# Performance work log

Measured on AMD Instinct MI355X. Metric: run time of the kernel, lower is better.

Reference implementation:

```python
import jax, jax.numpy as jnp
import numpy as np
import math

D_MODEL = 768
H = 12
D_FF = 3072
HEAD_DIM = D_MODEL // H
EPS = 1e-5


def setup_inputs() -> dict:
    key = jax.random.key(0)
    ks = jax.random.split(key, 12)
    s = 1.0 / math.sqrt(D_MODEL)
    inp = {
        "x": jax.random.normal(ks[0], (8, 1024, D_MODEL), dtype=jnp.float32),
        # attention projections (stored as [d_in, d_out])
        "wq": jax.random.normal(ks[1], (D_MODEL, D_MODEL), jnp.float32) * s,
        "bq": jnp.zeros((D_MODEL,), jnp.float32),
        "wk": jax.random.normal(ks[2], (D_MODEL, D_MODEL), jnp.float32) * s,
        "bk": jnp.zeros((D_MODEL,), jnp.float32),
        "wv": jax.random.normal(ks[3], (D_MODEL, D_MODEL), jnp.float32) * s,
        "bv": jnp.zeros((D_MODEL,), jnp.float32),
        "wo": jax.random.normal(ks[4], (D_MODEL, D_MODEL), jnp.float32) * s,
        "bo": jnp.zeros((D_MODEL,), jnp.float32),
        # FFN
        "w1": jax.random.normal(ks[5], (D_MODEL, D_FF), jnp.float32) * s,
        "b1": jnp.zeros((D_FF,), jnp.float32),
        "w2": jax.random.normal(ks[6], (D_FF, D_MODEL), jnp.float32) * (1.0 / math.sqrt(D_FF)),
        "b2": jnp.zeros((D_MODEL,), jnp.float32),
        # LayerNormalization scalar params (gemma/beta) for the two residual norms
        "g1": jnp.ones((1,), jnp.float32),
        "be1": jnp.zeros((1,), jnp.float32),
        "g2": jnp.ones((1,), jnp.float32),
        "be2": jnp.zeros((1,), jnp.float32),
    }
    return inp


def _layernorm(x, g, b):
    # torch: mean and UNBIASED std over last dim; divide by (std + eps)
    mean = jnp.mean(x, axis=-1, keepdims=True)
    std = jnp.std(x, axis=-1, keepdims=True, ddof=1)
    return g * (x - mean) / (std + EPS) + b


def _attention(x, wq, bq, wk, bk, wv, bv, wo, bo):
    B, N, _ = x.shape
    q = (x @ wq + bq).reshape(B, N, H, HEAD_DIM)
    k = (x @ wk + bk).reshape(B, N, H, HEAD_DIM)
    v = (x @ wv + bv).reshape(B, N, H, HEAD_DIM)
    scores = jnp.einsum("bqhd,bkhd->bhqk", q, k) / math.sqrt(HEAD_DIM)
    w = jax.nn.softmax(scores, axis=-1)
    out = jnp.einsum("bhqk,bkhd->bqhd", w, v).reshape(B, N, D_MODEL)
    return out @ wo + bo


def _ffn(x, w1, b1, w2, b2):
    return (jax.nn.gelu(x @ w1 + b1, approximate=False)) @ w2 + b2


def reference(x, wq, bq, wk, bk, wv, bv, wo, bo, w1, b1, w2, b2, g1, be1, g2, be2):
    # pre-LN residual block 1: attention
    x = x + _attention(_layernorm(x, g1, be1), wq, bq, wk, bk, wv, bv, wo, bo)
    # pre-LN residual block 2: FFN
    x = x + _ffn(_layernorm(x, g2, be2), w1, b1, w2, b2)
    return x
```

## Files before the change

### kernel.cpp

```cpp
#include <hip/hip_runtime.h>
#include <hip/hip_bf16.h>
#include <math.h>

typedef unsigned short u16;
typedef unsigned int u32;
typedef u16 u16x8 __attribute__((ext_vector_type(8)));
typedef __bf16 bf16x8 __attribute__((ext_vector_type(8)));
typedef float f32x4 __attribute__((ext_vector_type(4)));

#define MODE_GELU 1
#define MODE_RESF32 2
#define MODE_QKV 3

template <typename T, typename F>
__device__ __forceinline__ T bitcast(F f) { return __builtin_bit_cast(T, f); }

__device__ __forceinline__ u16 f2bf(float f) {
    unsigned int u = __float_as_uint(f);
    u = (u + 0x7fffu + ((u >> 16) & 1u)) >> 16;
    return (u16)u;
}

__device__ __forceinline__ u32 packbf(float lo, float hi) {
    return (u32)f2bf(lo) | ((u32)f2bf(hi) << 16);
}

__device__ __forceinline__ float fast_gelu(float x) {
    const float arg = x * (2.30220775f + 0.10294329f * x * x);
    const float e = exp2f(arg);
    return x * (1.0f - __builtin_amdgcn_rcpf(e + 1.0f));
}

__device__ __forceinline__ void gl_lds16(const u16* g, u16* l) {
    __builtin_amdgcn_global_load_lds(
        (const __attribute__((address_space(1))) unsigned int*)(const void*)g,
        (__attribute__((address_space(3))) unsigned int*)(void*)l,
        16, 0, 0);
}

__device__ __forceinline__ void stage64(const u16* __restrict__ src, int stride,
                                        u16* __restrict__ lds, int t)
{
    const int wave = t >> 6, lane = t & 63;
#pragma unroll
    for (int i = 0; i < 2; i++) {
        const int row = i * 32 + wave * 8 + (lane >> 3);
        const int s = lane & 7;
        const int f = (((row >> 3) & 1) << 2) | (row & 3);
        gl_lds16(src + (size_t)row * stride + (size_t)((s ^ f) << 3),
                 lds + i * 2048 + wave * 512);
    }
}

__global__ __launch_bounds__(256) void prep_kernel(
    const float* __restrict__ wq, const float* __restrict__ wk,
    const float* __restrict__ wv, const float* __restrict__ wo,
    const float* __restrict__ w1, const float* __restrict__ w2,
    const float* __restrict__ bq, const float* __restrict__ bk,
    const float* __restrict__ bv,
    u16* __restrict__ wqkvT, u16* __restrict__ woT,
    u16* __restrict__ w1T, u16* __restrict__ w2T, float* __restrict__ bqkv,
    const float* __restrict__ X, u16* __restrict__ Y,
    const float* __restrict__ gp, const float* __restrict__ bp)
{
    const int blk = blockIdx.x;
    if (blk >= 6921) {
        __shared__ float sbuf[8];
        const int row = blk - 6921, t = threadIdx.x;
        const float* xr = X + (size_t)row * 768;
        float v0 = xr[t], v1 = xr[t + 256], v2 = xr[t + 512];
        float s = v0 + v1 + v2;
        float q = v0 * v0 + v1 * v1 + v2 * v2;
#pragma unroll
        for (int m = 1; m < 64; m <<= 1) {
            s += __shfl_xor(s, m, 64);
            q += __shfl_xor(q, m, 64);
        }
        const int wave = t >> 6, lane = t & 63;
        if (lane == 0) { sbuf[wave] = s; sbuf[4 + wave] = q; }
        __syncthreads();
        s = sbuf[0] + sbuf[1] + sbuf[2] + sbuf[3];
        q = sbuf[4] + sbuf[5] + sbuf[6] + sbuf[7];
        const float mean = s * (1.0f / 768.0f);
        float ssd = fmaxf(q - 768.0f * mean * mean, 0.0f);
        const float stdv = sqrtf(ssd * (1.0f / 767.0f));
        const float scale = gp[0] / (stdv + 1e-5f);
        const float beta = bp[0];
        u16* yr = Y + (size_t)row * 768;
        yr[t]       = f2bf((v0 - mean) * scale + beta);
        yr[t + 256] = f2bf((v1 - mean) * scale + beta);
        yr[t + 512] = f2bf((v2 - mean) * scale + beta);
        return;
    }
    if (blk >= 6912) {
        const int t = (blk - 6912) * 256 + threadIdx.x;
        if (t < 2304)
            bqkv[t] = t < 768 ? bq[t] : (t < 1536 ? bk[t - 768] : bv[t - 1536]);
        return;
    }
    const float* W; u16* WT; int Krows, Ncols, lt;
    if (blk < 576)       { W = wq; WT = wqkvT;                       Krows = 768;  Ncols = 768;  lt = blk; }
    else if (blk < 1152) { W = wk; WT = wqkvT + (size_t)768 * 768;   Krows = 768;  Ncols = 768;  lt = blk - 576; }
    else if (blk < 1728) { W = wv; WT = wqkvT + (size_t)1536 * 768;  Krows = 768;  Ncols = 768;  lt = blk - 1152; }
    else if (blk < 2304) { W = wo; WT = woT;                         Krows = 768;  Ncols = 768;  lt = blk - 1728; }
    else if (blk < 4608) { W = w1; WT = w1T;                         Krows = 768;  Ncols = 3072; lt = blk - 2304; }
    else                 { W = w2; WT = w2T;                         Krows = 3072; Ncols = 768;  lt = blk - 4608; }
    const int ktiles = Krows >> 5;
    const int k0 = (lt % ktiles) * 32, n0 = (lt / ktiles) * 32;

    __shared__ float tile[32][33];
    const int tx = threadIdx.x & 31, ty = threadIdx.x >> 5;
#pragma unroll
    for (int j = 0; j < 32; j += 8)
        tile[ty + j][tx] = W[(size_t)(k0 + ty + j) * Ncols + n0 + tx];
    __syncthreads();
#pragma unroll
    for (int j = 0; j < 32; j += 8)
        WT[(size_t)(n0 + ty + j) * Krows + k0 + tx] = f2bf(tile[tx][ty + j]);
}

__global__ __launch_bounds__(256) void ln_kernel(
    const float* __restrict__ X, u16* __restrict__ Y,
    const float* __restrict__ gp, const float* __restrict__ bp)
{
    __shared__ float sbuf[8];
    const int row = blockIdx.x, t = threadIdx.x;
    const float* xr = X + (size_t)row * 768;
    float v0 = xr[t], v1 = xr[t + 256], v2 = xr[t + 512];
    float s = v0 + v1 + v2;
    float q = v0 * v0 + v1 * v1 + v2 * v2;
#pragma unroll
    for (int m = 1; m < 64; m <<= 1) {
        s += __shfl_xor(s, m, 64);
        q += __shfl_xor(q, m, 64);
    }
    const int wave = t >> 6, lane = t & 63;
    if (lane == 0) { sbuf[wave] = s; sbuf[4 + wave] = q; }
    __syncthreads();
    s = sbuf[0] + sbuf[1] + sbuf[2] + sbuf[3];
    q = sbuf[4] + sbuf[5] + sbuf[6] + sbuf[7];
    const float mean = s * (1.0f / 768.0f);
    float ssd = fmaxf(q - 768.0f * mean * mean, 0.0f);
    const float stdv = sqrtf(ssd * (1.0f / 767.0f));
    const float scale = gp[0] / (stdv + 1e-5f);
    const float beta = bp[0];
    u16* yr = Y + (size_t)row * 768;
    yr[t]       = f2bf((v0 - mean) * scale + beta);
    yr[t + 256] = f2bf((v1 - mean) * scale + beta);
    yr[t + 512] = f2bf((v2 - mean) * scale + beta);
}

template <int MODE>
__global__ __launch_bounds__(256) void gemm_kernel(
    const u16* __restrict__ A, const u16* __restrict__ BT,
    const float* __restrict__ bias, const float* __restrict__ res,
    void* __restrict__ out0, void* __restrict__ out1, void* __restrict__ out2,
    int M, int N, int K)
{
    __shared__ u16 sh[2][2][128 * 64];
    u16* shp = &sh[0][0][0];
    const int t = threadIdx.x;
    const int lane = t & 63, wave = t >> 6;
    const int wr = wave >> 1, wc = wave & 1;
    const int g = lane >> 4, c = lane & 15;
    const int bm = blockIdx.x, bn = blockIdx.y;

    const int srow = wave * 32 + (lane >> 3);
    const u16* Ag = A + (size_t)(bm * 128 + srow) * K;
    const u16* Bg = BT + (size_t)(bn * 128 + srow) * K;

    const int fc = (((c >> 3) & 1) << 2) | (c & 3);
    const int xs0 = (g ^ fc) << 3;
    const int xs1 = ((4 + g) ^ fc) << 3;

    f32x4 acc[4][4] = {};
    const int nk = K >> 6;

    const int sl = lane & 7;
    int sco[4];
#pragma unroll
    for (int it = 0; it < 4; it++)
        sco[it] = ((sl ^ (((it & 1) << 2) | ((lane >> 3) & 3))) << 3);

#define STAGE_AB(buf, k0)                                                     \
    {                                                                         \
        _Pragma("unroll")                                                     \
        for (int it = 0; it < 4; it++) {                                      \
            gl_lds16(Ag + (size_t)(it * 8) * K + (k0) + sco[it], &sh[buf][0][wave * 2048 + it * 512]); \
            gl_lds16(Bg + (size_t)(it * 8) * K + (k0) + sco[it], &sh[buf][1][wave * 2048 + it * 512]); \
        }                                                                     \
    }

    STAGE_AB(0, 0);
    __syncthreads();

    for (int ks = 0; ks < nk; ks++) {
        const int cur = ks & 1;
        if (ks + 1 < nk) STAGE_AB(cur ^ 1, (ks + 1) << 6);
        const u16* Asb = sh[cur][0];
        const u16* Bsb = sh[cur][1];
        __builtin_amdgcn_s_setprio(1);
#pragma unroll
        for (int kk = 0; kk < 2; kk++) {
            const int xo = kk ? xs1 : xs0;
            bf16x8 af[4], bfr[4];
#pragma unroll
            for (int m = 0; m < 4; m++)
                af[m] = *(const bf16x8*)&Asb[(wr * 64 + m * 16 + c) * 64 + xo];
#pragma unroll
            for (int n = 0; n < 4; n++)
                bfr[n] = *(const bf16x8*)&Bsb[(wc * 64 + n * 16 + c) * 64 + xo];
#pragma unroll
            for (int m = 0; m < 4; m++)
#pragma unroll
                for (int n = 0; n < 4; n++)
                    acc[m][n] = __builtin_amdgcn_mfma_f32_16x16x32_bf16(
                        af[m], bfr[n], acc[m][n], 0, 0, 0);
        }
        __builtin_amdgcn_s_setprio(0);
        __syncthreads();
    }
#undef STAGE_AB

    if constexpr (MODE == MODE_QKV) {
        if (bn >= 12) {
#pragma unroll
            for (int m = 0; m < 4; m++) {
#pragma unroll
                for (int n = 0; n < 4; n++) {
                    const int colL = wc * 64 + n * 16 + c;
                    const int rowLb = wr * 64 + m * 16 + 4 * g;
                    const float bv = bias[bn * 128 + colL];
                    const u32 x0 = packbf(acc[m][n][0] + bv, acc[m][n][1] + bv);
                    const u32 x1 = packbf(acc[m][n][2] + bv, acc[m][n][3] + bv);
                    const int elem = colL * 128 + (rowLb ^ ((colL & 15) << 3));
                    ((u32*)shp)[elem >> 1] = x0;
                    ((u32*)shp)[(elem >> 1) + 1] = x1;
                }
            }
            __syncthreads();
            const int bn_off = bn - 12;
            const int bb = bm >> 3, kvb = (bm & 7) * 128;
            const int j8 = (t & 7) * 8;
#pragma unroll
            for (int it = 0; it < 4; it++) {
                const int colL2 = it * 32 + (t >> 3);
                const int gcol = bn_off * 128 + colL2;
                const int hh = gcol >> 6, d = gcol & 63;
                const size_t obase = ((size_t)(bb * 12 + hh) << 16) + ((size_t)d << 10) + kvb;
                const int X = (colL2 & 15) << 3;
#pragma unroll
                for (int half = 0; half < 2; half++) {
                    const int rowL2 = half * 64 + j8;
                    const int elem = colL2 * 128 + (rowL2 ^ X);
                    *(u16x8*)((u16*)out2 + obase + rowL2) = *(const u16x8*)&shp[elem];
                }
            }
            return;
        }
    }

#pragma unroll
    for (int m = 0; m < 4; m++) {
        const int row = bm * 128 + wr * 64 + m * 16 + 4 * g;
#pragma unroll
        for (int n = 0; n < 4; n++) {
            const int col = bn * 128 + wc * 64 + n * 16 + c;
            const float bv = bias[col];
#pragma unroll
            for (int i = 0; i < 4; i++) {
                float v = acc[m][n][i] + bv;
                if constexpr (MODE == MODE_GELU) {
                    ((u16*)out0)[(size_t)(row + i) * N + col] = f2bf(fast_gelu(v));
                } else if constexpr (MODE == MODE_RESF32) {
                    const size_t idx = (size_t)(row + i) * N + col;
                    ((float*)out0)[idx] = v + res[idx];
                } else {
                    const int sect = (col >= 768) ? 1 : 0;
                    const int colm = col - sect * 768;
                    u16* dst = sect ? (u16*)out1 : (u16*)out0;
                    dst[(size_t)(row + i) * 768 + colm] = f2bf(v);
                }
            }
        }
    }
}

__global__ __launch_bounds__(256) void attn_kernel(
    const u16* __restrict__ Qg, const u16* __restrict__ Kg,
    const u16* __restrict__ Vt_g, u16* __restrict__ O)
{
    __shared__ u16 Kl[2][4096];
    __shared__ u16 Vl[2][4096];
    const int t = threadIdx.x, lane = t & 63, wave = t >> 6;
    const int g = lane >> 4, c = lane & 15;
    const int l = blockIdx.x;
    const int pos = l >> 3;
    const int b = l & 7, h = pos >> 4;
    const int qt = pos & 15;
    const int bh = b * 12 + h;
    const size_t rowb = (size_t)b * 1024;
    const int q0 = qt * 64 + wave * 16;

    bf16x8 qa[2];
    {
        const u16* qp = Qg + (rowb + q0 + c) * 768 + h * 64 + g * 8;
        u16x8 a0 = *(const u16x8*)qp;
        u16x8 a1 = *(const u16x8*)(qp + 32);
        bf16x8 va0, va1;
#pragma unroll
        for (int j = 0; j < 8; j++) {
            const float SC = 0.18033688011112042f;
            va0[j] = (__bf16)(__uint_as_float(((u32)a0[j]) << 16) * SC);
            va1[j] = (__bf16)(__uint_as_float(((u32)a1[j]) << 16) * SC);
        }
        qa[0] = va0; qa[1] = va1;
    }

    int kro[4], kxo[4], vro[4];
#pragma unroll
    for (int n = 0; n < 4; n++) {
        const int pr = ((n >> 1) << 5) + ((c >> 2) << 3) + ((n & 1) << 2) + (c & 3);
        kro[n] = pr << 6;
        kxo[n] = (((pr >> 3) & 1) << 2) | (pr & 3);
        vro[n] = (n * 16 + c) << 6;
    }
    const int vxo = (((c >> 3) & 1) << 2) | (c & 3);

    const u16* ksrc = Kg + rowb * 768 + h * 64;
    const u16* vsrc = Vt_g + (size_t)bh * 65536;

    float m0 = -1e30f, l0 = 0.f;
    f32x4 oa[4] = {};
    const int srcb = (lane & 48) | ((lane >> 2) & 12);

    stage64(ksrc, 768, Kl[0], t);
    stage64(vsrc, 1024, Vl[0], t);
    __syncthreads();

    for (int kvt = 0; kvt < 16; ++kvt) {
        const u16* Kc = Kl[kvt & 1];
        const u16* Vc = Vl[kvt & 1];
        if (kvt < 15) {
            stage64(ksrc + (size_t)(kvt + 1) * 64 * 768, 768, Kl[(kvt + 1) & 1], t);
            stage64(vsrc + (kvt + 1) * 64, 1024, Vl[(kvt + 1) & 1], t);
        }

        f32x4 s0[4] = {};
        __builtin_amdgcn_s_setprio(1);
#pragma unroll
        for (int n = 0; n < 4; n++) {
#pragma unroll
            for (int kk = 0; kk < 2; kk++) {
                const bf16x8 kf = *(const bf16x8*)&Kc[kro[n] + ((((kk << 2) + g) ^ kxo[n]) << 3)];
                s0[n] = __builtin_amdgcn_mfma_f32_16x16x32_bf16(kf, qa[kk], s0[n], 0, 0, 0);
            }
        }
        __builtin_amdgcn_s_setprio(0);

        bf16x8 pa00, pa01;
        {
            float t0 = fmaxf(fmaxf(s0[0][0], s0[0][1]), fmaxf(s0[0][2], s0[0][3]));
            float t1 = fmaxf(fmaxf(s0[1][0], s0[1][1]), fmaxf(s0[1][2], s0[1][3]));
            float t2 = fmaxf(fmaxf(s0[2][0], s0[2][1]), fmaxf(s0[2][2], s0[2][3]));
            float t3 = fmaxf(fmaxf(s0[3][0], s0[3][1]), fmaxf(s0[3][2], s0[3][3]));
            float mx = fmaxf(fmaxf(t0, t1), fmaxf(t2, t3));
            mx = fmaxf(mx, __shfl_xor(mx, 16, 64));
            mx = fmaxf(mx, __shfl_xor(mx, 32, 64));
            if (!__all(mx <= m0 + 8.0f)) {
                const float mn = fmaxf(m0, mx);
                const float rsc = exp2f(m0 - mn);
                m0 = mn; l0 *= rsc;
                f32x4 rq;
#pragma unroll
                for (int i = 0; i < 4; i++) rq[i] = __shfl(rsc, srcb + i, 64);
#pragma unroll
                for (int n = 0; n < 4; n++) oa[n] *= rq;
            }
            float r = 0.f;
#pragma unroll
            for (int n = 0; n < 4; n++)
#pragma unroll
                for (int i = 0; i < 4; i++) {
                    s0[n][i] = exp2f(s0[n][i] - m0);
                    r += s0[n][i];
                }
            r += __shfl_xor(r, 16, 64);
            r += __shfl_xor(r, 32, 64);
            l0 += r;
#pragma unroll
            for (int i = 0; i < 4; i++) {
                pa00[i] = (__bf16)s0[0][i]; pa00[4 + i] = (__bf16)s0[1][i];
                pa01[i] = (__bf16)s0[2][i]; pa01[4 + i] = (__bf16)s0[3][i];
            }
        }

        __builtin_amdgcn_s_setprio(1);
#pragma unroll
        for (int n = 0; n < 4; n++) {
#pragma unroll
            for (int kk = 0; kk < 2; kk++) {
                const bf16x8 vf = *(const bf16x8*)&Vc[vro[n] + ((((kk << 2) + g) ^ vxo) << 3)];
                oa[n] = __builtin_amdgcn_mfma_f32_16x16x32_bf16(kk ? pa01 : pa00, vf, oa[n], 0, 0, 0);
            }
        }
        __builtin_amdgcn_s_setprio(0);
        __syncthreads();
    }

#pragma unroll
    for (int i = 0; i < 4; i++) {
        const float la = __shfl(l0, srcb + i, 64);
        const float ia_ = 1.0f / fmaxf(la, 1e-30f);
        const size_t ra_ = rowb + q0 + 4 * g + i;
#pragma unroll
        for (int n = 0; n < 4; n++)
            O[ra_ * 768 + h * 64 + n * 16 + c] = f2bf(oa[n][i] * ia_);
    }
}

extern "C" void kernel_launch(void* const* d_in, const int* in_sizes, int n_in,
                              void* d_out, int out_size, void* d_ws, size_t ws_size,
                              hipStream_t stream)
{
    const float* x   = (const float*)d_in[0];
    const float* wq  = (const float*)d_in[1];
    const float* bq  = (const float*)d_in[2];
    const float* wk  = (const float*)d_in[3];
    const float* bk  = (const float*)d_in[4];
    const float* wv  = (const float*)d_in[5];
    const float* bv  = (const float*)d_in[6];
    const float* wo  = (const float*)d_in[7];
    const float* bo  = (const float*)d_in[8];
    const float* w1  = (const float*)d_in[9];
    const float* b1  = (const float*)d_in[10];
    const float* w2  = (const float*)d_in[11];
    const float* b2  = (const float*)d_in[12];
    const float* g1  = (const float*)d_in[13];
    const float* be1 = (const float*)d_in[14];
    const float* g2  = (const float*)d_in[15];
    const float* be2 = (const float*)d_in[16];

    char* ws = (char*)d_ws;
    constexpr size_t O_WQKV = 0;
    constexpr size_t O_WO   = 3538944;
    constexpr size_t O_W1   = 4718592;
    constexpr size_t O_W2   = 9437184;
    constexpr size_t O_BQKV = 14155776;
    constexpr size_t O_XLN  = 14168064;
    constexpr size_t O_Q    = O_XLN + 12582912;
    constexpr size_t O_K    = O_Q + 12582912;
    constexpr size_t O_VT   = O_K + 12582912;
    constexpr size_t O_ATTN = O_VT + 12582912;
    constexpr size_t O_H    = O_ATTN + 12582912;
    constexpr size_t O_F    = O_XLN;
    constexpr size_t O_HLN  = O_ATTN;

    u16* wqkvT = (u16*)(ws + O_WQKV);
    u16* woT   = (u16*)(ws + O_WO);
    u16* w1T   = (u16*)(ws + O_W1);
    u16* w2T   = (u16*)(ws + O_W2);
    float* bqkv = (float*)(ws + O_BQKV);
    u16* xln   = (u16*)(ws + O_XLN);
    u16* Qb    = (u16*)(ws + O_Q);
    u16* Kb    = (u16*)(ws + O_K);
    u16* VTg   = (u16*)(ws + O_VT);
    u16* attnb = (u16*)(ws + O_ATTN);
    float* h   = (float*)(ws + O_H);
    u16* fb    = (u16*)(ws + O_F);
    u16* hln   = (u16*)(ws + O_HLN);

    dim3 blk(256);
    prep_kernel<<<6921 + 8192, blk, 0, stream>>>(wq, wk, wv, wo, w1, w2, bq, bk, bv,
                                                 wqkvT, woT, w1T, w2T, bqkv,
                                                 x, xln, g1, be1);
    gemm_kernel<MODE_QKV><<<dim3(64, 18), blk, 0, stream>>>(
        xln, wqkvT, bqkv, nullptr, Qb, Kb, VTg, 8192, 2304, 768);
    attn_kernel<<<1536, blk, 0, stream>>>(Qb, Kb, VTg, attnb);
    gemm_kernel<MODE_RESF32><<<dim3(64, 6), blk, 0, stream>>>(
        attnb, woT, bo, x, h, nullptr, nullptr, 8192, 768, 768);
    ln_kernel<<<8192, blk, 0, stream>>>(h, hln, g2, be2);
    gemm_kernel<MODE_GELU><<<dim3(64, 24), blk, 0, stream>>>(
        hln, w1T, b1, nullptr, fb, nullptr, nullptr, 8192, 3072, 768);
    gemm_kernel<MODE_RESF32><<<dim3(64, 6), blk, 0, stream>>>(
        fb, w2T, b2, h, (float*)d_out, nullptr, nullptr, 8192, 768, 3072);
}
```

Measured before the change: 242.5 us.

## Compute softmax row sums via MFMA with ones vector and swizzle GEMM block order

The attention kernel now accumulates the softmax denominator with two extra MFMAs against a ones vector, taking the row sums of the bf16 probabilities. This replaces the per-tile scalar adds and cross-lane shuffle reductions. The max reduction is rewritten as a linear chain, and the GEMM remaps block indices so that consecutive blocks on each XCD share M-tiles, for better L2 reuse. The denominator now sums the bf16-rounded values, which matches the numerator more closely but changes numerics slightly.

```diff
diff --git a/kernel.cpp b/kernel.cpp
--- a/kernel.cpp
+++ b/kernel.cpp
@@ -163,7 +163,11 @@
     const int lane = t & 63, wave = t >> 6;
     const int wr = wave >> 1, wc = wave & 1;
     const int g = lane >> 4, c = lane & 15;
-    const int bm = blockIdx.x, bn = blockIdx.y;
+
+    const int lin = blockIdx.x + blockIdx.y * gridDim.x;
+    const int xcd = lin & 7, idx = lin >> 3;
+    const int bm = xcd * 8 + (idx & 7);
+    const int bn = idx >> 3;
 
     const int srow = wave * 32 + (lane >> 3);
     const u16* Ag = A + (size_t)(bm * 128 + srow) * K;
@@ -317,6 +321,10 @@
         qa[0] = va0; qa[1] = va1;
     }
 
+    bf16x8 vone;
+#pragma unroll
+    for (int j = 0; j < 8; j++) vone[j] = (__bf16)1.0f;
+
     int kro[4], kxo[4], vro[4];
 #pragma unroll
     for (int n = 0; n < 4; n++) {
@@ -330,8 +338,9 @@
     const u16* ksrc = Kg + rowb * 768 + h * 64;
     const u16* vsrc = Vt_g + (size_t)bh * 65536;
 
-    float m0 = -1e30f, l0 = 0.f;
+    float m0 = -1e30f;
     f32x4 oa[4] = {};
+    f32x4 lsum = {};
     const int srcb = (lane & 48) | ((lane >> 2) & 12);
 
     stage64(ksrc, 768, Kl[0], t);
@@ -360,34 +369,32 @@
 
         bf16x8 pa00, pa01;
         {
-            float t0 = fmaxf(fmaxf(s0[0][0], s0[0][1]), fmaxf(s0[0][2], s0[0][3]));
-            float t1 = fmaxf(fmaxf(s0[1][0], s0[1][1]), fmaxf(s0[1][2], s0[1][3]));
-            float t2 = fmaxf(fmaxf(s0[2][0], s0[2][1]), fmaxf(s0[2][2], s0[2][3]));
-            float t3 = fmaxf(fmaxf(s0[3][0], s0[3][1]), fmaxf(s0[3][2], s0[3][3]));
-            float mx = fmaxf(fmaxf(t0, t1), fmaxf(t2, t3));
+            float mx = fmaxf(fmaxf(s0[0][0], s0[0][1]), s0[0][2]);
+            mx = fmaxf(fmaxf(mx, s0[0][3]), s0[1][0]);
+            mx = fmaxf(fmaxf(mx, s0[1][1]), s0[1][2]);
+            mx = fmaxf(fmaxf(mx, s0[1][3]), s0[2][0]);
+            mx = fmaxf(fmaxf(mx, s0[2][1]), s0[2][2]);
+            mx = fmaxf(fmaxf(mx, s0[2][3]), s0[3][0]);
+            mx = fmaxf(fmaxf(mx, s0[3][1]), s0[3][2]);
+            mx = fmaxf(mx, s0[3][3]);
             mx = fmaxf(mx, __shfl_xor(mx, 16, 64));
             mx = fmaxf(mx, __shfl_xor(mx, 32, 64));
             if (!__all(mx <= m0 + 8.0f)) {
                 const float mn = fmaxf(m0, mx);
                 const float rsc = exp2f(m0 - mn);
-                m0 = mn; l0 *= rsc;
+                m0 = mn;
                 f32x4 rq;
 #pragma unroll
                 for (int i = 0; i < 4; i++) rq[i] = __shfl(rsc, srcb + i, 64);
 #pragma unroll
                 for (int n = 0; n < 4; n++) oa[n] *= rq;
-            }
-            float r = 0.f;
+                lsum *= rq;
+            }
 #pragma unroll
             for (int n = 0; n < 4; n++)
 #pragma unroll
-                for (int i = 0; i < 4; i++) {
+                for (int i = 0; i < 4; i++)
                     s0[n][i] = exp2f(s0[n][i] - m0);
-                    r += s0[n][i];
-                }
-            r += __shfl_xor(r, 16, 64);
-            r += __shfl_xor(r, 32, 64);
-            l0 += r;
 #pragma unroll
             for (int i = 0; i < 4; i++) {
                 pa00[i] = (__bf16)s0[0][i]; pa00[4 + i] = (__bf16)s0[1][i];
@@ -396,6 +403,8 @@
         }
 
         __builtin_amdgcn_s_setprio(1);
+        lsum = __builtin_amdgcn_mfma_f32_16x16x32_bf16(pa00, vone, lsum, 0, 0, 0);
+        lsum = __builtin_amdgcn_mfma_f32_16x16x32_bf16(pa01, vone, lsum, 0, 0, 0);
 #pragma unroll
         for (int n = 0; n < 4; n++) {
 #pragma unroll
@@ -410,8 +419,7 @@
 
 #pragma unroll
     for (int i = 0; i < 4; i++) {
-        const float la = __shfl(l0, srcb + i, 64);
-        const float ia_ = 1.0f / fmaxf(la, 1e-30f);
+        const float ia_ = 1.0f / fmaxf(lsum[i], 1e-30f);
         const size_t ra_ = rowb + q0 + 4 * g + i;
 #pragma unroll
         for (int n = 0; n < 4; n++)
```

Measured after the change: 237.7 us. -2.0%, faster.
